# Kernel optimization log

Measured on AMD Instinct MI355X. Metric: run time of the kernel, lower is better.

## Reference

```python
import jax, jax.numpy as jnp
import numpy as np

B = 8192
COND_DIM = 64
OUT_DIM = 64      # output_dim (joint velocity dim)
ACT_DIM = 8       # action_dim (latent action dim)
H1, H2 = 256, 256


def setup_inputs() -> dict:
    key = jax.random.key(0)
    ks = jax.random.split(key, 8)
    inp = {
        "cond_inp": jax.random.normal(ks[0], (B, COND_DIM), dtype=jnp.float32),
        "low_level_action": jax.random.normal(ks[1], (B, OUT_DIM), dtype=jnp.float32),
        # MLP params: cond_dim -> 256 -> 256 -> action_dim*output_dim
        "W1": jax.random.normal(ks[2], (COND_DIM, H1), dtype=jnp.float32) / np.sqrt(COND_DIM),
        "b1": jnp.zeros((H1,), dtype=jnp.float32),
        "W2": jax.random.normal(ks[3], (H1, H2), dtype=jnp.float32) / np.sqrt(H1),
        "b2": jnp.zeros((H2,), dtype=jnp.float32),
        "W3": jax.random.normal(ks[4], (H2, ACT_DIM * OUT_DIM), dtype=jnp.float32) / np.sqrt(H2),
        "b3": jnp.zeros((ACT_DIM * OUT_DIM,), dtype=jnp.float32),
    }
    return inp


def _householder(Hcols):
    # Hcols: [B, n, k]; chain of k batched Householder reflections.
    n = Hcols.shape[1]
    k = Hcols.shape[2]
    I = jnp.eye(n, dtype=Hcols.dtype)
    Q = jnp.broadcast_to(I, (Hcols.shape[0], n, n))
    for c in range(k):  # small fixed unroll over latent action columns
        v = Hcols[:, :, c]                                  # [B, n]
        vvT = jnp.einsum('bi,bj->bij', v, v)                # [B, n, n]
        vTv = jnp.einsum('bi,bi->b', v, v)[:, None, None]   # [B, 1, 1]
        Qi = I - 2.0 * vvT / vTv
        Q = jnp.matmul(Qi, Q)
    return Q[:, :, :k]


def reference(cond_inp, low_level_action, W1, b1, W2, b2, W3, b3):
    # MLP h(cond_inp)
    x = jnp.tanh(cond_inp @ W1 + b1)
    x = jnp.tanh(x @ W2 + b2)
    x = x @ W3 + b3                                    # [B, act*out]
    Hcols = x.reshape(-1, OUT_DIM, ACT_DIM)            # [B, out, act]
    scl_map = _householder(Hcols)                      # [B, out, act], orthonormal cols
    # best action: a* = S^T qdot ; reconstruction: qdot_hat = S a*
    a_star = jnp.einsum('bnk,bn->bk', scl_map, low_level_action)   # [B, act]
    q_dot_hat = jnp.einsum('bnk,bk->bn', scl_map, a_star)          # [B, out]
    return q_dot_hat[..., None]                        # [B, out, 1] (matches tf.matmul shape)
```

## Files before the change

kernel.cpp:

```cpp
#include <hip/hip_runtime.h>

typedef float f4 __attribute__((ext_vector_type(4)));
typedef float f2 __attribute__((ext_vector_type(2)));
typedef float f32x4 __attribute__((ext_vector_type(4)));
typedef _Float16 f16x8 __attribute__((ext_vector_type(8)));

#define HSWZ16(o) ((o) ^ (((o) >> 3) & 0x70))

#define BARLG() asm volatile("s_waitcnt lgkmcnt(0)\n\ts_barrier" ::: "memory")

__global__ __launch_bounds__(256) void prep_frags_all(
    const float* __restrict__ W1, const float* __restrict__ W2,
    const float* __restrict__ W3, _Float16* __restrict__ dst) {
    __shared__ float s[32 * 264];
    const int b = blockIdx.x, tid = threadIdx.x;
    const float* W; int N, kt, nh, KT; size_t off;
    if (b < 2)       { W = W1; N = 256; KT = 2; kt = b;            nh = 0;          off = 0; }
    else if (b < 10) { W = W2; N = 256; KT = 8; kt = b - 2;        nh = 0;          off = 16384; }
    else             { W = W3; N = 512; KT = 8; kt = (b - 10) >> 1; nh = (b - 10) & 1; off = 81920; }
    #pragma unroll
    for (int rep = 0; rep < 8; ++rep) {
        int fi = rep * 256 + tid;
        int row = fi >> 6, c4 = fi & 63;
        f4 v = *(const f4*)&W[(kt * 32 + row) * N + nh * 256 + c4 * 4];
        *(f4*)&s[row * 264 + c4 * 4] = v;
    }
    __syncthreads();
    const int wv = tid >> 6, l = tid & 63, lr = l & 15, lg = l >> 4;
    #pragma unroll
    for (int p = 0; p < 4; ++p) {
        int lnt = wv * 4 + p;
        f16x8 o;
        #pragma unroll
        for (int j = 0; j < 8; ++j)
            o[j] = (_Float16)s[(lg * 8 + j) * 264 + lnt * 16 + lr];
        int page = (nh * 16 + lnt) * KT + kt;
        *(f16x8*)&dst[off + (size_t)page * 512 + l * 8] = o;
    }
}

__device__ __forceinline__ float ftanh(float x) {
    float e = __expf(2.0f * x);
    return 1.0f - 2.0f / (e + 1.0f);
}
__device__ __forceinline__ float red32(float x) {
    x += __shfl_xor(x, 1); x += __shfl_xor(x, 2);  x += __shfl_xor(x, 4);
    x += __shfl_xor(x, 8); x += __shfl_xor(x, 16);
    return x;
}

__global__ __launch_bounds__(512, 4) void scl_mfma(
    const float* __restrict__ cond, const float* __restrict__ act,
    const float* __restrict__ b1, const float* __restrict__ b2,
    const float* __restrict__ b3,
    const _Float16* __restrict__ wf,
    float* __restrict__ out)
{
    __shared__ char smem[33792];
    _Float16* x1h = (_Float16*)smem;
    _Float16* x1l = (_Float16*)(smem + 8448);
    _Float16* x2h = (_Float16*)(smem + 16896);
    _Float16* x2l = (_Float16*)(smem + 25344);

    const int tid = threadIdx.x;
    const int w   = tid >> 6;
    const int l   = tid & 63;
    const int lr  = l & 15;
    const int lg  = l >> 4;
    const int rb  = blockIdx.x * 16;
    const f16x8* wp = (const f16x8*)wf;

    const int hrow = w * 2 + (l >> 5), hc = l & 31;
    f2 av = *(const f2*)&act[(rb + hrow) * 64 + 2 * hc];
    const float* crow = cond + (rb + lr) * 64 + lg * 8;
    f4 c0a = *(const f4*)crow;
    f4 c0b = *(const f4*)(crow + 4);
    f4 c1a = *(const f4*)(crow + 32);
    f4 c1b = *(const f4*)(crow + 36);
    f16x8 w1f[2][2];
    #pragma unroll
    for (int n = 0; n < 2; ++n)
        #pragma unroll
        for (int kt = 0; kt < 2; ++kt)
            w1f[n][kt] = wp[((w * 2 + n) * 2 + kt) * 64 + l];
    f16x8 w2f[2][8];
    #pragma unroll
    for (int n = 0; n < 2; ++n)
        #pragma unroll
        for (int kt = 0; kt < 8; ++kt)
            w2f[n][kt] = wp[2048 + ((w * 2 + n) * 8 + kt) * 64 + l];
    float b1v[2], b2v[2], b3v[4];
    #pragma unroll
    for (int n = 0; n < 2; ++n) {
        b1v[n] = b1[(w * 2 + n) * 16 + lr];
        b2v[n] = b2[(w * 2 + n) * 16 + lr];
    }
    #pragma unroll
    for (int n = 0; n < 4; ++n) b3v[n] = b3[(w * 4 + n) * 16 + lr];

    {
        float v0[8] = {c0a[0], c0a[1], c0a[2], c0a[3], c0b[0], c0b[1], c0b[2], c0b[3]};
        float v1[8] = {c1a[0], c1a[1], c1a[2], c1a[3], c1b[0], c1b[1], c1b[2], c1b[3]};
        f16x8 ah[2], al[2];
        #pragma unroll
        for (int j = 0; j < 8; ++j) {
            _Float16 h0 = (_Float16)v0[j];
            ah[0][j] = h0; al[0][j] = (_Float16)(v0[j] - (float)h0);
            _Float16 h1 = (_Float16)v1[j];
            ah[1][j] = h1; al[1][j] = (_Float16)(v1[j] - (float)h1);
        }
        f32x4 acc[2] = {};
        #pragma unroll
        for (int n = 0; n < 2; ++n)
            #pragma unroll
            for (int kt = 0; kt < 2; ++kt) {
                acc[n] = __builtin_amdgcn_mfma_f32_16x16x32_f16(ah[kt], w1f[n][kt], acc[n], 0, 0, 0);
                acc[n] = __builtin_amdgcn_mfma_f32_16x16x32_f16(al[kt], w1f[n][kt], acc[n], 0, 0, 0);
            }
        #pragma unroll
        for (int n = 0; n < 2; ++n) {
            int col = (w * 2 + n) * 16 + lr;
            #pragma unroll
            for (int r = 0; r < 4; ++r) {
                float v = ftanh(acc[n][r] + b1v[n]);
                int row = lg * 4 + r;
                _Float16 hx = (_Float16)v;
                x1h[row * 264 + col] = hx;
                x1l[row * 264 + col] = (_Float16)(v - (float)hx);
            }
        }
    }
    BARLG();

    f16x8 w3f[4][8];
    #pragma unroll
    for (int n = 0; n < 4; ++n)
        #pragma unroll
        for (int kt = 0; kt < 4; ++kt)
            w3f[n][kt] = wp[10240 + ((w * 4 + n) * 8 + kt) * 64 + l];
    {
        f32x4 acc[2] = {};
        #pragma unroll
        for (int kt = 0; kt < 8; ++kt) {
            int cb = kt * 32 + lg * 8;
            f16x8 ah = *(const f16x8*)&x1h[lr * 264 + cb];
            f16x8 al = *(const f16x8*)&x1l[lr * 264 + cb];
            #pragma unroll
            for (int n = 0; n < 2; ++n) {
                acc[n] = __builtin_amdgcn_mfma_f32_16x16x32_f16(ah, w2f[n][kt], acc[n], 0, 0, 0);
                acc[n] = __builtin_amdgcn_mfma_f32_16x16x32_f16(al, w2f[n][kt], acc[n], 0, 0, 0);
            }
        }
        #pragma unroll
        for (int n = 0; n < 2; ++n) {
            int col = (w * 2 + n) * 16 + lr;
            #pragma unroll
            for (int r = 0; r < 4; ++r) {
                float v = ftanh(acc[n][r] + b2v[n]);
                int row = lg * 4 + r;
                _Float16 hx = (_Float16)v;
                x2h[row * 264 + col] = hx;
                x2l[row * 264 + col] = (_Float16)(v - (float)hx);
            }
        }
    }
    BARLG();

    #pragma unroll
    for (int n = 0; n < 4; ++n)
        #pragma unroll
        for (int kt = 4; kt < 8; ++kt)
            w3f[n][kt] = wp[10240 + ((w * 4 + n) * 8 + kt) * 64 + l];
    {
        f32x4 acc[4] = {};
        #pragma unroll
        for (int kt = 0; kt < 8; ++kt) {
            int cb = kt * 32 + lg * 8;
            f16x8 ah = *(const f16x8*)&x2h[lr * 264 + cb];
            f16x8 al = *(const f16x8*)&x2l[lr * 264 + cb];
            #pragma unroll
            for (int n = 0; n < 4; ++n) {
                acc[n] = __builtin_amdgcn_mfma_f32_16x16x32_f16(ah, w3f[n][kt], acc[n], 0, 0, 0);
                acc[n] = __builtin_amdgcn_mfma_f32_16x16x32_f16(al, w3f[n][kt], acc[n], 0, 0, 0);
            }
        }
        #pragma unroll
        for (int n = 0; n < 4; ++n) {
            int col = (w * 4 + n) * 16 + lr;
            #pragma unroll
            for (int r = 0; r < 4; ++r) {
                int row = lg * 4 + r;
                *(_Float16*)(smem + row * 1056 + HSWZ16(col * 2)) = (_Float16)(acc[n][r] + b3v[n]);
            }
        }
    }
    BARLG();

    {
        f16x8 hv[2];
        #pragma unroll
        for (int j = 0; j < 2; ++j)
            hv[j] = *(const f16x8*)(smem + hrow * 1056 + HSWZ16(hc * 32 + j * 16));
        float h[8][2];
        #pragma unroll
        for (int cc = 0; cc < 8; ++cc) {
            h[cc][0] = (float)hv[0][cc];
            h[cc][1] = (float)hv[1][cc];
        }
        float inv[8];
        #pragma unroll
        for (int cc = 0; cc < 8; ++cc) {
            float s = h[cc][0] * h[cc][0] + h[cc][1] * h[cc][1];
            inv[cc] = 2.0f / red32(s);
        }
        float u[2] = {av[0], av[1]};
        #pragma unroll
        for (int cc = 7; cc >= 0; --cc) {
            float d = red32(h[cc][0] * u[0] + h[cc][1] * u[1]);
            float t = inv[cc] * d;
            u[0] -= t * h[cc][0];
            u[1] -= t * h[cc][1];
        }
        float wv[2];
        wv[0] = (hc < 4) ? u[0] : 0.0f;
        wv[1] = (hc < 4) ? u[1] : 0.0f;
        #pragma unroll
        for (int cc = 0; cc < 8; ++cc) {
            float d = red32(h[cc][0] * wv[0] + h[cc][1] * wv[1]);
            float t = inv[cc] * d;
            wv[0] -= t * h[cc][0];
            wv[1] -= t * h[cc][1];
        }
        f2 o = {wv[0], wv[1]};
        *(f2*)&out[(rb + hrow) * 64 + 2 * hc] = o;
    }
}

extern "C" void kernel_launch(void* const* d_in, const int* in_sizes, int n_in,
                              void* d_out, int out_size, void* d_ws, size_t ws_size,
                              hipStream_t stream) {
    const float* cond = (const float*)d_in[0];
    const float* act  = (const float*)d_in[1];
    const float* W1   = (const float*)d_in[2];
    const float* b1   = (const float*)d_in[3];
    const float* W2   = (const float*)d_in[4];
    const float* b2   = (const float*)d_in[5];
    const float* W3   = (const float*)d_in[6];
    const float* b3   = (const float*)d_in[7];
    float* outp = (float*)d_out;

    _Float16* wf = (_Float16*)d_ws;
    prep_frags_all<<<dim3(26), dim3(256), 0, stream>>>(W1, W2, W3, wf);
    scl_mfma<<<dim3(512), dim3(512), 0, stream>>>(cond, act, b1, b2, b3, wf, outp);
}
```

Before: 26.61 us.

## Drop fp16 split precision, use 32-row blocks of 1024 threads, 8-lane Householder

Removes the hi/lo fp16 split of the activations, so each GEMM stage issues half as many MFMAs and needs half the LDS traffic. Blocks now hold 32 rows and 16 waves, and each wave owns one 16-column slice of layers 1 and 2 and two of layer 3, so each weight fragment is reused across two row tiles. The Householder stage is remapped to 8 lanes per row with 8 elements each, which needs only 3-step shuffle reductions, but only 4 of the 16 waves do that work. The cost is lower precision from single fp16 activations and a larger block with idle waves in the final stage.

Measured after the change: 25.51 us, median of 2. -4.1%, faster.

```diff
diff --git a/kernel.cpp b/kernel.cpp
--- a/kernel.cpp
+++ b/kernel.cpp
@@ -1,7 +1,6 @@
 #include <hip/hip_runtime.h>
 
 typedef float f4 __attribute__((ext_vector_type(4)));
-typedef float f2 __attribute__((ext_vector_type(2)));
 typedef float f32x4 __attribute__((ext_vector_type(4)));
 typedef _Float16 f16x8 __attribute__((ext_vector_type(8)));
 
@@ -43,13 +42,12 @@
     float e = __expf(2.0f * x);
     return 1.0f - 2.0f / (e + 1.0f);
 }
-__device__ __forceinline__ float red32(float x) {
-    x += __shfl_xor(x, 1); x += __shfl_xor(x, 2);  x += __shfl_xor(x, 4);
-    x += __shfl_xor(x, 8); x += __shfl_xor(x, 16);
+__device__ __forceinline__ float red8(float x) {
+    x += __shfl_xor(x, 1); x += __shfl_xor(x, 2); x += __shfl_xor(x, 4);
     return x;
 }
 
-__global__ __launch_bounds__(512, 4) void scl_mfma(
+__global__ __launch_bounds__(1024, 4) void scl_mfma(
     const float* __restrict__ cond, const float* __restrict__ act,
     const float* __restrict__ b1, const float* __restrict__ b2,
     const float* __restrict__ b3,
@@ -57,182 +55,188 @@
     float* __restrict__ out)
 {
     __shared__ char smem[33792];
-    _Float16* x1h = (_Float16*)smem;
-    _Float16* x1l = (_Float16*)(smem + 8448);
-    _Float16* x2h = (_Float16*)(smem + 16896);
-    _Float16* x2l = (_Float16*)(smem + 25344);
+    _Float16* x1 = (_Float16*)smem;
+    _Float16* x2 = (_Float16*)(smem + 16896);
 
     const int tid = threadIdx.x;
     const int w   = tid >> 6;
     const int l   = tid & 63;
     const int lr  = l & 15;
     const int lg  = l >> 4;
-    const int rb  = blockIdx.x * 16;
+    const int rb  = blockIdx.x * 32;
     const f16x8* wp = (const f16x8*)wf;
 
-    const int hrow = w * 2 + (l >> 5), hc = l & 31;
-    f2 av = *(const f2*)&act[(rb + hrow) * 64 + 2 * hc];
-    const float* crow = cond + (rb + lr) * 64 + lg * 8;
-    f4 c0a = *(const f4*)crow;
-    f4 c0b = *(const f4*)(crow + 4);
-    f4 c1a = *(const f4*)(crow + 32);
-    f4 c1b = *(const f4*)(crow + 36);
-    f16x8 w1f[2][2];
-    #pragma unroll
-    for (int n = 0; n < 2; ++n)
-        #pragma unroll
-        for (int kt = 0; kt < 2; ++kt)
-            w1f[n][kt] = wp[((w * 2 + n) * 2 + kt) * 64 + l];
-    f16x8 w2f[2][8];
-    #pragma unroll
-    for (int n = 0; n < 2; ++n)
-        #pragma unroll
-        for (int kt = 0; kt < 8; ++kt)
-            w2f[n][kt] = wp[2048 + ((w * 2 + n) * 8 + kt) * 64 + l];
-    float b1v[2], b2v[2], b3v[4];
-    #pragma unroll
-    for (int n = 0; n < 2; ++n) {
-        b1v[n] = b1[(w * 2 + n) * 16 + lr];
-        b2v[n] = b2[(w * 2 + n) * 16 + lr];
-    }
-    #pragma unroll
-    for (int n = 0; n < 4; ++n) b3v[n] = b3[(w * 4 + n) * 16 + lr];
-
-    {
-        float v0[8] = {c0a[0], c0a[1], c0a[2], c0a[3], c0b[0], c0b[1], c0b[2], c0b[3]};
-        float v1[8] = {c1a[0], c1a[1], c1a[2], c1a[3], c1b[0], c1b[1], c1b[2], c1b[3]};
-        f16x8 ah[2], al[2];
-        #pragma unroll
-        for (int j = 0; j < 8; ++j) {
-            _Float16 h0 = (_Float16)v0[j];
-            ah[0][j] = h0; al[0][j] = (_Float16)(v0[j] - (float)h0);
-            _Float16 h1 = (_Float16)v1[j];
-            ah[1][j] = h1; al[1][j] = (_Float16)(v1[j] - (float)h1);
-        }
-        f32x4 acc[2] = {};
-        #pragma unroll
-        for (int n = 0; n < 2; ++n)
-            #pragma unroll
-            for (int kt = 0; kt < 2; ++kt) {
-                acc[n] = __builtin_amdgcn_mfma_f32_16x16x32_f16(ah[kt], w1f[n][kt], acc[n], 0, 0, 0);
-                acc[n] = __builtin_amdgcn_mfma_f32_16x16x32_f16(al[kt], w1f[n][kt], acc[n], 0, 0, 0);
-            }
-        #pragma unroll
-        for (int n = 0; n < 2; ++n) {
-            int col = (w * 2 + n) * 16 + lr;
-            #pragma unroll
-            for (int r = 0; r < 4; ++r) {
-                float v = ftanh(acc[n][r] + b1v[n]);
-                int row = lg * 4 + r;
-                _Float16 hx = (_Float16)v;
-                x1h[row * 264 + col] = hx;
-                x1l[row * 264 + col] = (_Float16)(v - (float)hx);
-            }
-        }
-    }
-    BARLG();
-
-    f16x8 w3f[4][8];
-    #pragma unroll
-    for (int n = 0; n < 4; ++n)
-        #pragma unroll
-        for (int kt = 0; kt < 4; ++kt)
-            w3f[n][kt] = wp[10240 + ((w * 4 + n) * 8 + kt) * 64 + l];
+    f16x8 a1[2][2];
+    #pragma unroll
+    for (int m = 0; m < 2; ++m) {
+        const float* crow = cond + (rb + m * 16 + lr) * 64 + lg * 8;
+        #pragma unroll
+        for (int kt = 0; kt < 2; ++kt) {
+            f4 va = *(const f4*)(crow + kt * 32);
+            f4 vb = *(const f4*)(crow + kt * 32 + 4);
+            #pragma unroll
+            for (int j = 0; j < 4; ++j) {
+                a1[m][kt][j]     = (_Float16)va[j];
+                a1[m][kt][4 + j] = (_Float16)vb[j];
+            }
+        }
+    }
+    f16x8 w1f[2];
+    #pragma unroll
+    for (int kt = 0; kt < 2; ++kt) w1f[kt] = wp[(w * 2 + kt) * 64 + l];
+    f16x8 w2f[8];
+    #pragma unroll
+    for (int kt = 0; kt < 8; ++kt) w2f[kt] = wp[2048 + (w * 8 + kt) * 64 + l];
+    float b1v = b1[w * 16 + lr];
+    float b2v = b2[w * 16 + lr];
+    float b3v[2];
+    #pragma unroll
+    for (int n = 0; n < 2; ++n) b3v[n] = b3[(w * 2 + n) * 16 + lr];
+
+    f4 av0 = {}, av1 = {};
+    if (w < 4) {
+        const float* ap = act + (rb + w * 8 + (l >> 3)) * 64 + (l & 7) * 8;
+        av0 = *(const f4*)ap;
+        av1 = *(const f4*)(ap + 4);
+    }
+
     {
         f32x4 acc[2] = {};
         #pragma unroll
+        for (int kt = 0; kt < 2; ++kt)
+            #pragma unroll
+            for (int m = 0; m < 2; ++m)
+                acc[m] = __builtin_amdgcn_mfma_f32_16x16x32_f16(a1[m][kt], w1f[kt], acc[m], 0, 0, 0);
+        #pragma unroll
+        for (int m = 0; m < 2; ++m)
+            #pragma unroll
+            for (int r = 0; r < 4; ++r) {
+                float v = ftanh(acc[m][r] + b1v);
+                x1[(m * 16 + lg * 4 + r) * 264 + w * 16 + lr] = (_Float16)v;
+            }
+    }
+    BARLG();
+
+    f16x8 w3a[2][4];
+    #pragma unroll
+    for (int n = 0; n < 2; ++n)
+        #pragma unroll
+        for (int kt = 0; kt < 4; ++kt)
+            w3a[n][kt] = wp[10240 + ((w * 2 + n) * 8 + kt) * 64 + l];
+    {
+        f32x4 acc[2] = {};
+        #pragma unroll
         for (int kt = 0; kt < 8; ++kt) {
             int cb = kt * 32 + lg * 8;
-            f16x8 ah = *(const f16x8*)&x1h[lr * 264 + cb];
-            f16x8 al = *(const f16x8*)&x1l[lr * 264 + cb];
-            #pragma unroll
-            for (int n = 0; n < 2; ++n) {
-                acc[n] = __builtin_amdgcn_mfma_f32_16x16x32_f16(ah, w2f[n][kt], acc[n], 0, 0, 0);
-                acc[n] = __builtin_amdgcn_mfma_f32_16x16x32_f16(al, w2f[n][kt], acc[n], 0, 0, 0);
-            }
-        }
+            f16x8 am0 = *(const f16x8*)&x1[lr * 264 + cb];
+            f16x8 am1 = *(const f16x8*)&x1[(16 + lr) * 264 + cb];
+            acc[0] = __builtin_amdgcn_mfma_f32_16x16x32_f16(am0, w2f[kt], acc[0], 0, 0, 0);
+            acc[1] = __builtin_amdgcn_mfma_f32_16x16x32_f16(am1, w2f[kt], acc[1], 0, 0, 0);
+        }
+        #pragma unroll
+        for (int m = 0; m < 2; ++m)
+            #pragma unroll
+            for (int r = 0; r < 4; ++r) {
+                float v = ftanh(acc[m][r] + b2v);
+                x2[(m * 16 + lg * 4 + r) * 264 + w * 16 + lr] = (_Float16)v;
+            }
+    }
+    BARLG();
+
+    f16x8 w3b[2][4];
+    #pragma unroll
+    for (int n = 0; n < 2; ++n)
+        #pragma unroll
+        for (int kt = 0; kt < 4; ++kt)
+            w3b[n][kt] = wp[10240 + ((w * 2 + n) * 8 + (kt + 4)) * 64 + l];
+    f32x4 acc3[2][2] = {};
+    #pragma unroll
+    for (int kt = 0; kt < 4; ++kt) {
+        int cb = kt * 32 + lg * 8;
+        f16x8 am0 = *(const f16x8*)&x2[lr * 264 + cb];
+        f16x8 am1 = *(const f16x8*)&x2[(16 + lr) * 264 + cb];
         #pragma unroll
         for (int n = 0; n < 2; ++n) {
-            int col = (w * 2 + n) * 16 + lr;
+            acc3[0][n] = __builtin_amdgcn_mfma_f32_16x16x32_f16(am0, w3a[n][kt], acc3[0][n], 0, 0, 0);
+            acc3[1][n] = __builtin_amdgcn_mfma_f32_16x16x32_f16(am1, w3a[n][kt], acc3[1][n], 0, 0, 0);
+        }
+    }
+    #pragma unroll
+    for (int kt = 4; kt < 8; ++kt) {
+        int cb = kt * 32 + lg * 8;
+        f16x8 am0 = *(const f16x8*)&x2[lr * 264 + cb];
+        f16x8 am1 = *(const f16x8*)&x2[(16 + lr) * 264 + cb];
+        #pragma unroll
+        for (int n = 0; n < 2; ++n) {
+            acc3[0][n] = __builtin_amdgcn_mfma_f32_16x16x32_f16(am0, w3b[n][kt - 4], acc3[0][n], 0, 0, 0);
+            acc3[1][n] = __builtin_amdgcn_mfma_f32_16x16x32_f16(am1, w3b[n][kt - 4], acc3[1][n], 0, 0, 0);
+        }
+    }
+    BARLG();
+
+    #pragma unroll
+    for (int n = 0; n < 2; ++n) {
+        int col = (w * 2 + n) * 16 + lr;
+        #pragma unroll
+        for (int m = 0; m < 2; ++m)
             #pragma unroll
             for (int r = 0; r < 4; ++r) {
-                float v = ftanh(acc[n][r] + b2v[n]);
-                int row = lg * 4 + r;
-                _Float16 hx = (_Float16)v;
-                x2h[row * 264 + col] = hx;
-                x2l[row * 264 + col] = (_Float16)(v - (float)hx);
-            }
-        }
-    }
-    BARLG();
-
-    #pragma unroll
-    for (int n = 0; n < 4; ++n)
-        #pragma unroll
-        for (int kt = 4; kt < 8; ++kt)
-            w3f[n][kt] = wp[10240 + ((w * 4 + n) * 8 + kt) * 64 + l];
-    {
-        f32x4 acc[4] = {};
-        #pragma unroll
-        for (int kt = 0; kt < 8; ++kt) {
-            int cb = kt * 32 + lg * 8;
-            f16x8 ah = *(const f16x8*)&x2h[lr * 264 + cb];
-            f16x8 al = *(const f16x8*)&x2l[lr * 264 + cb];
-            #pragma unroll
-            for (int n = 0; n < 4; ++n) {
-                acc[n] = __builtin_amdgcn_mfma_f32_16x16x32_f16(ah, w3f[n][kt], acc[n], 0, 0, 0);
-                acc[n] = __builtin_amdgcn_mfma_f32_16x16x32_f16(al, w3f[n][kt], acc[n], 0, 0, 0);
-            }
-        }
-        #pragma unroll
-        for (int n = 0; n < 4; ++n) {
-            int col = (w * 4 + n) * 16 + lr;
-            #pragma unroll
-            for (int r = 0; r < 4; ++r) {
-                int row = lg * 4 + r;
-                *(_Float16*)(smem + row * 1056 + HSWZ16(col * 2)) = (_Float16)(acc[n][r] + b3v[n]);
-            }
-        }
-    }
-    BARLG();
-
-    {
-        f16x8 hv[2];
-        #pragma unroll
-        for (int j = 0; j < 2; ++j)
-            hv[j] = *(const f16x8*)(smem + hrow * 1056 + HSWZ16(hc * 32 + j * 16));
-        float h[8][2];
+                int row = m * 16 + lg * 4 + r;
+                *(_Float16*)(smem + row * 1056 + HSWZ16(col * 2)) =
+                    (_Float16)(acc3[m][n][r] + b3v[n]);
+            }
+    }
+    BARLG();
+
+    if (w < 4) {
+        const int c = l & 7;
+        const int hrow = w * 8 + (l >> 3);
+        const int grow = rb + hrow;
+        f16x8 hv[8];
+        #pragma unroll
+        for (int j = 0; j < 8; ++j)
+            hv[j] = *(const f16x8*)(smem + hrow * 1056 + HSWZ16((c * 8 + j) * 16));
+        float h[8][8];
+        #pragma unroll
+        for (int cc = 0; cc < 8; ++cc)
+            #pragma unroll
+            for (int j = 0; j < 8; ++j)
+                h[cc][j] = (float)hv[j][cc];
+        float inv[8];
         #pragma unroll
         for (int cc = 0; cc < 8; ++cc) {
-            h[cc][0] = (float)hv[0][cc];
-            h[cc][1] = (float)hv[1][cc];
-        }
-        float inv[8];
+            float s = 0.0f;
+            #pragma unroll
+            for (int j = 0; j < 8; ++j) s += h[cc][j] * h[cc][j];
+            inv[cc] = 2.0f / red8(s);
+        }
+        float u[8] = {av0[0], av0[1], av0[2], av0[3], av1[0], av1[1], av1[2], av1[3]};
+        #pragma unroll
+        for (int cc = 7; cc >= 0; --cc) {
+            float d = 0.0f;
+            #pragma unroll
+            for (int j = 0; j < 8; ++j) d += h[cc][j] * u[j];
+            float t = inv[cc] * red8(d);
+            #pragma unroll
+            for (int j = 0; j < 8; ++j) u[j] -= t * h[cc][j];
+        }
+        float wv[8];
+        #pragma unroll
+        for (int j = 0; j < 8; ++j) wv[j] = (c == 0) ? u[j] : 0.0f;
         #pragma unroll
         for (int cc = 0; cc < 8; ++cc) {
-            float s = h[cc][0] * h[cc][0] + h[cc][1] * h[cc][1];
-            inv[cc] = 2.0f / red32(s);
-        }
-        float u[2] = {av[0], av[1]};
-        #pragma unroll
-        for (int cc = 7; cc >= 0; --cc) {
-            float d = red32(h[cc][0] * u[0] + h[cc][1] * u[1]);
-            float t = inv[cc] * d;
-            u[0] -= t * h[cc][0];
-            u[1] -= t * h[cc][1];
-        }
-        float wv[2];
-        wv[0] = (hc < 4) ? u[0] : 0.0f;
-        wv[1] = (hc < 4) ? u[1] : 0.0f;
-        #pragma unroll
-        for (int cc = 0; cc < 8; ++cc) {
-            float d = red32(h[cc][0] * wv[0] + h[cc][1] * wv[1]);
-            float t = inv[cc] * d;
-            wv[0] -= t * h[cc][0];
-            wv[1] -= t * h[cc][1];
-        }
-        f2 o = {wv[0], wv[1]};
-        *(f2*)&out[(rb + hrow) * 64 + 2 * hc] = o;
+            float d = 0.0f;
+            #pragma unroll
+            for (int j = 0; j < 8; ++j) d += h[cc][j] * wv[j];
+            float t = inv[cc] * red8(d);
+            #pragma unroll
+            for (int j = 0; j < 8; ++j) wv[j] -= t * h[cc][j];
+        }
+        f4 o0 = {wv[0], wv[1], wv[2], wv[3]};
+        f4 o1 = {wv[4], wv[5], wv[6], wv[7]};
+        float* op = out + grow * 64 + c * 8;
+        *(f4*)op = o0;
+        *(f4*)(op + 4) = o1;
     }
 }
 
@@ -251,5 +255,5 @@
 
     _Float16* wf = (_Float16*)d_ws;
     prep_frags_all<<<dim3(26), dim3(256), 0, stream>>>(W1, W2, W3, wf);
-    scl_mfma<<<dim3(512), dim3(512), 0, stream>>>(cond, act, b1, b2, b3, wf, outp);
-}
+    scl_mfma<<<dim3(256), dim3(1024), 0, stream>>>(cond, act, b1, b2, b3, wf, outp);
+}
```
